# Kernel tuning notes

Measured on AMD Instinct MI355X. Metric: run time of the kernel, lower is better.

The kernel has to match this reference:

```python
import jax, jax.numpy as jnp
import numpy as np

B, S, H, I = 2, 4096, 2048, 8192
K_RATIO = 0.5
K = int(K_RATIO * I)  # 4096 kept activations per token


def setup_inputs() -> dict:
    key = jax.random.key(0)
    kx, kg, ku, kd = jax.random.split(key, 4)
    x = jax.random.normal(kx, (B, S, H), dtype=jnp.float32)
    # nn.Linear(in, out, bias=False) weight has shape [out, in]; y = x @ W.T
    Wg = jax.random.normal(kg, (I, H), dtype=jnp.float32) * (1.0 / np.sqrt(H))
    Wu = jax.random.normal(ku, (I, H), dtype=jnp.float32) * (1.0 / np.sqrt(H))
    Wd = jax.random.normal(kd, (H, I), dtype=jnp.float32) * (1.0 / np.sqrt(I))
    return {"x": x, "Wg": Wg, "Wu": Wu, "Wd": Wd}


def topk_activation(g):
    # Keep top-K entries by magnitude along the last dim, zero the rest.
    ag = jnp.abs(g)
    kth = jax.lax.top_k(ag, K)[0][..., -1:]  # [B,S,1] k-th largest |g|
    return jnp.where(ag >= kth, g, jnp.zeros_like(g))


def reference(x, Wg, Wu, Wd):
    gate = topk_activation(jnp.einsum('bsh,ih->bsi', x, Wg))  # [B,S,I] sparse
    up = jnp.einsum('bsh,ih->bsi', x, Wu)                      # [B,S,I]
    return jnp.einsum('bsi,hi->bsh', gate * up, Wd)            # [B,S,H]
```

## Files before the change

### kernel.cpp

```cpp
#include <hip/hip_runtime.h>

#define T_TOK 8192
#define HDIM  2048
#define IDIM  8192
#define KKEEP 4096
#define TCHK  4096
#define BAND  1.6e-3f
#define MAXB  192

typedef _Float16 f16x8 __attribute__((ext_vector_type(8)));
typedef float    f32x4 __attribute__((ext_vector_type(4)));
typedef ushort   u16x8 __attribute__((ext_vector_type(8)));

#define AS1 __attribute__((address_space(1)))
#define AS3 __attribute__((address_space(3)))
#define BARR asm volatile("s_barrier" ::: "memory")

__device__ __forceinline__ int swzA(int b) {
    return b ^ ((b >> 3) & 0x30) ^ ((b >> 2) & 0x40);
}

union H16 { ushort u; _Float16 h; };


__global__ void cast_f16(const float4* __restrict__ in, ushort4* __restrict__ o, long n4) {
    long stride = (long)gridDim.x * blockDim.x;
    for (long i = (long)blockIdx.x * blockDim.x + threadIdx.x; i < n4; i += stride) {
        float4 v = in[i];
        float vv[4] = {v.x, v.y, v.z, v.w};
        union { _Float16 f[4]; ushort4 u; } H;
        #pragma unroll
        for (int j = 0; j < 4; ++j) H.f[j] = (_Float16)vv[j];
        o[i] = H.u;
    }
}

#define GLOAD(src_, dst_) \
    __builtin_amdgcn_global_load_lds((const AS1 void*)(src_), (AS3 void*)(dst_), 16, 0, 0)


#define STAGE4(pA_, pB_, kt_, buf_) do { \
    char* db_ = Lc + (buf_)*32768 + wave*1024; \
    GLOAD((pA_) + aBase + (kt_) + off0, db_); \
    GLOAD((pA_) + aBase + (kt_) + off1, db_ +  8192); \
    GLOAD((pB_) + bBase + (kt_) + off2, db_ + 16384); \
    GLOAD((pB_) + bBase + (kt_) + off3, db_ + 24576); \
  } while (0)

#define RDFRAG(dstA_, dstB_, tt_) do { \
    const char* bp_ = Lc + ((tt_) & 3) * 32768; \
    _Pragma("unroll") \
    for (int m_ = 0; m_ < 8; ++m_) (dstA_)[m_] = *(const f16x8*)(bp_ + pa + m_ * 1024); \
    _Pragma("unroll") \
    for (int n_ = 0; n_ < 4; ++n_) (dstB_)[n_] = *(const f16x8*)(bp_ + pb + n_ * 1024); \
  } while (0)

#define BODY(t_, curA_, curB_, nxtA_, nxtB_) do { \
    if ((t_) + 2 < NT) asm volatile("s_waitcnt vmcnt(4)" ::: "memory"); \
    else               asm volatile("s_waitcnt vmcnt(0)" ::: "memory"); \
    BARR; \
    if ((t_) + 3 < NT) STAGE4(A0, B0, ((t_) + 3) << 5, ((t_) + 3) & 3); \
    if ((t_) + 1 < NT) RDFRAG(nxtA_, nxtB_, (t_) + 1); \
    __builtin_amdgcn_s_setprio(1); \
    _Pragma("unroll") \
    for (int m_ = 0; m_ < 8; ++m_) \
      _Pragma("unroll") \
      for (int n_ = 0; n_ < 4; ++n_) \
        acc[m_][n_] = __builtin_amdgcn_mfma_f32_16x16x32_f16((curA_)[m_], (curB_)[n_], acc[m_][n_], 0, 0, 0); \
    __builtin_amdgcn_s_setprio(0); \
  } while (0)

template <int MODE>
__global__ __launch_bounds__(512, 2) void gemm4(
    const _Float16* __restrict__ A0, const _Float16* __restrict__ B0,
    int N, int Kp, float* __restrict__ Cf, _Float16* __restrict__ Ch)
{
    __shared__ __align__(128) char Lc[131072];
    const int tid  = threadIdx.x;
    const int lane = tid & 63;
    const int wave = tid >> 6;
    const int wr = wave >> 2, wc = wave & 3;

    const int gx = gridDim.x, gy = gridDim.y;
    const int nwg = gx * gy;
    const int orig = blockIdx.y * gx + blockIdx.x;
    const int q = nwg >> 3, r = nwg & 7, xcd = orig & 7, lid = orig >> 3;
    const int wg = (xcd < r ? xcd * (q + 1) : r * (q + 1) + (xcd - r) * q) + lid;
    const int bm = wg / gy, bn = wg % gy;

    int off0, off1, off2, off3;
    {
        int o[4];
        #pragma unroll
        for (int g = 0; g < 4; ++g) {
            int p = g * 8192 + tid * 16;
            int l = swzA(p);
            int row = (l >> 6) & 255;
            int col = (l & 63) >> 1;
            o[g] = row * Kp + col;
        }
        off0 = o[0]; off1 = o[1]; off2 = o[2]; off3 = o[3];
    }
    const size_t aBase = (size_t)bm * 256 * Kp;
    const size_t bBase = (size_t)bn * 256 * Kp;

    const int l15 = lane & 15, lhi = lane >> 4;
    const int pa = swzA((wr * 128 + l15) * 64 + lhi * 16);
    const int pb = swzA(16384 + (wc * 64 + l15) * 64 + lhi * 16);

    const int NT = Kp >> 5;
    f32x4 acc[8][4] = {};
    f16x8 a0f[8], b0f[4], a1f[8], b1f[4];

    STAGE4(A0, B0, 0,  0);
    STAGE4(A0, B0, 32, 1);
    STAGE4(A0, B0, 64, 2);
    asm volatile("s_waitcnt vmcnt(8)" ::: "memory");
    BARR;
    RDFRAG(a0f, b0f, 0);

    for (int t = 0; t < NT; t += 2) {
        BODY(t,     a0f, b0f, a1f, b1f);
        BODY(t + 1, a1f, b1f, a0f, b0f);
    }

    const int r0 = bm * 256 + wr * 128 + (lane >> 4) * 4;
    const int c0 = bn * 256 + wc * 64 + (lane & 15);
    #pragma unroll
    for (int m = 0; m < 8; ++m) {
        #pragma unroll
        for (int n = 0; n < 4; ++n) {
            #pragma unroll
            for (int rr = 0; rr < 4; ++rr) {
                const size_t idx = (size_t)(r0 + m * 16 + rr) * N + (c0 + n * 16);
                if (MODE == 0) Cf[idx] = acc[m][n][rr];
                else           Ch[idx] = (_Float16)acc[m][n][rr];
            }
        }
    }
}


__global__ __launch_bounds__(256) void topk_sel(
    _Float16* __restrict__ GP, const _Float16* __restrict__ U,
    const float* __restrict__ xf, const float* __restrict__ Wgf)
{
    __shared__ ushort keys[IDIM];
    __shared__ float  xrow[HDIM];
    __shared__ unsigned char bmap[IDIM];
    __shared__ unsigned hist[256], sA_[256], sB_[256];
    __shared__ unsigned selBin, selAbove;
    __shared__ int Acnt, nbv;
    __shared__ int   bidxs[MAXB];
    __shared__ float bval[MAXB];
    __shared__ int   kflag[MAXB];

    const int tid = threadIdx.x;
    const int t = blockIdx.x;
    _Float16* grow = GP + (size_t)t * IDIM;
    const _Float16* urow = U + (size_t)t * IDIM;

    if (tid == 0) { Acnt = 0; nbv = 0; }
    for (int j8 = tid * 8; j8 < IDIM; j8 += 2048) {
        u16x8 v = *(const u16x8*)(grow + j8);
        u16x8 k;
        #pragma unroll
        for (int e = 0; e < 8; ++e) k[e] = (ushort)(v[e] & 0x7FFFu);
        *(u16x8*)(keys + j8) = k;
    }
    for (int j4 = tid; j4 < IDIM / 4; j4 += 256)
        ((unsigned*)bmap)[j4] = 0xFFFFFFFFu;
    for (int j4 = tid * 4; j4 < HDIM; j4 += 1024)
        *(float4*)(xrow + j4) = *(const float4*)(xf + (size_t)t * HDIM + j4);
    __syncthreads();

    unsigned kq = 0;
    int Krem = KKEEP;
    for (int pass = 0; pass < 2; ++pass) {
        const int shift = pass == 0 ? 7 : 0;
        const unsigned msk = pass == 0 ? 255u : 127u;
        hist[tid] = 0;
        __syncthreads();
        for (int j8 = tid * 8; j8 < IDIM; j8 += 2048) {
            u16x8 kv = *(const u16x8*)(keys + j8);
            #pragma unroll
            for (int e = 0; e < 8; ++e) {
                unsigned k = kv[e];
                bool ok = (pass == 0) || ((k >> 7) == (kq >> 7));
                if (ok) atomicAdd(&hist[(k >> shift) & msk], 1u);
            }
        }
        __syncthreads();
        sA_[tid] = hist[tid];
        __syncthreads();
        unsigned *src = sA_, *dst = sB_;
        for (int off = 1; off < 256; off <<= 1) {
            unsigned v = src[tid] + ((tid + off < 256) ? src[tid + off] : 0u);
            dst[tid] = v;
            __syncthreads();
            unsigned* tmp = src; src = dst; dst = tmp;
        }
        unsigned S  = src[tid];
        unsigned Sn = (tid < 255) ? src[tid + 1] : 0u;
        if ((int)S >= Krem && (int)Sn < Krem) { selBin = (unsigned)tid; selAbove = Sn; }
        __syncthreads();
        kq |= selBin << shift;
        Krem -= (int)selAbove;
        __syncthreads();
    }
    H16 cv; cv.u = (ushort)kq;
    const float kthf = (float)cv.h;
    const float hif = kthf + BAND;
    const float lof = kthf - BAND;

    for (int j8 = tid * 8; j8 < IDIM; j8 += 2048) {
        u16x8 kv = *(const u16x8*)(keys + j8);
        #pragma unroll
        for (int e = 0; e < 8; ++e) {
            H16 c; c.u = kv[e];
            float v = (float)c.h;
            if (v > hif) atomicAdd(&Acnt, 1);
            else if (v >= lof) {
                int s = atomicAdd(&nbv, 1);
                if (s < MAXB) { bidxs[s] = j8 + e; bmap[j8 + e] = (unsigned char)s; }
            }
        }
    }
    __syncthreads();

    const int nbc = nbv < MAXB ? nbv : MAXB;
    int R = KKEEP - Acnt;
    R = R < 0 ? 0 : (R > nbc ? nbc : R);

    const int wv = tid >> 6, ln = tid & 63;
    for (int j = wv; j < nbc; j += 4) {
        const float* wrow = Wgf + (size_t)bidxs[j] * HDIM;
        float s = 0.f;
        #pragma unroll
        for (int it = 0; it < HDIM / 256; ++it) {
            const int c = it * 256 + ln * 4;
            float4 w = *(const float4*)(wrow + c);
            float4 xv = *(const float4*)(xrow + c);
            s = fmaf(xv.x, w.x, s);
            s = fmaf(xv.y, w.y, s);
            s = fmaf(xv.z, w.z, s);
            s = fmaf(xv.w, w.w, s);
        }
        #pragma unroll
        for (int o = 32; o; o >>= 1) s += __shfl_xor(s, o);
        if (ln == 0) bval[j] = fabsf(s);
    }
    __syncthreads();

    for (int j = tid; j < nbc; j += 256) {
        int rk = 0;
        float vj = bval[j];
        for (int k = 0; k < nbc; ++k) rk += (bval[k] > vj);
        kflag[j] = (rk < R) ? 1 : 0;
    }
    __syncthreads();

    for (int j8 = tid * 8; j8 < IDIM; j8 += 2048) {
        u16x8 g8 = *(const u16x8*)(grow + j8);
        u16x8 u8 = *(const u16x8*)(urow + j8);
        u16x8 p8;
        #pragma unroll
        for (int e = 0; e < 8; ++e) {
            H16 cg; cg.u = g8[e];
            H16 cu; cu.u = u8[e];
            float g = (float)cg.h;
            float v = fabsf(g);
            bool keep;
            unsigned char s = bmap[j8 + e];
            if (s != 255)      keep = (kflag[s] != 0);
            else if (v > hif)  keep = true;
            else if (v < lof)  keep = false;
            else               keep = (v >= kthf);
            H16 cp; cp.h = keep ? (_Float16)(g * (float)cu.h) : (_Float16)0.f;
            p8[e] = cp.u;
        }
        *(u16x8*)(grow + j8) = p8;
    }
}


extern "C" void kernel_launch(void* const* d_in, const int* in_sizes, int n_in,
                              void* d_out, int out_size, void* d_ws, size_t ws_size,
                              hipStream_t stream) {
    const float* x  = (const float*)d_in[0];
    const float* Wg = (const float*)d_in[1];
    const float* Wu = (const float*)d_in[2];
    const float* Wd = (const float*)d_in[3];

    const size_t NE   = (size_t)T_TOK * HDIM;
    const size_t szH2 = NE * 2;

    char* ws = (char*)d_ws;
    _Float16* xh   = (_Float16*)ws;
    _Float16* Wgh  = (_Float16*)(ws + szH2);
    _Float16* Wu16 = (_Float16*)(ws + 2 * szH2);
    _Float16* Wd16 = (_Float16*)(ws + 3 * szH2);
    _Float16* G    = (_Float16*)(ws + 4 * szH2);
    _Float16* Uc   = (_Float16*)d_out;

    const long n4 = (long)(NE / 4);
    cast_f16<<<1024, 256, 0, stream>>>((const float4*)x,  (ushort4*)xh,   n4);
    cast_f16<<<1024, 256, 0, stream>>>((const float4*)Wg, (ushort4*)Wgh,  n4);
    cast_f16<<<1024, 256, 0, stream>>>((const float4*)Wu, (ushort4*)Wu16, n4);
    cast_f16<<<1024, 256, 0, stream>>>((const float4*)Wd, (ushort4*)Wd16, n4);

    gemm4<1><<<dim3(T_TOK / 256, IDIM / 256), 512, 0, stream>>>(
        xh, Wgh, IDIM, HDIM, nullptr, G);

    for (int c0 = 0; c0 < T_TOK; c0 += TCHK) {
        gemm4<1><<<dim3(TCHK / 256, IDIM / 256), 512, 0, stream>>>(
            xh + (size_t)c0 * HDIM, Wu16, IDIM, HDIM, nullptr, Uc);
        topk_sel<<<TCHK, 256, 0, stream>>>(
            G + (size_t)c0 * IDIM, Uc, x + (size_t)c0 * HDIM, Wg);
    }

    gemm4<0><<<dim3(T_TOK / 256, HDIM / 256), 512, 0, stream>>>(
        G, Wd16, HDIM, IDIM, (float*)d_out, nullptr);
}
```

Measured before the change: 1.243 ms.

## Shrink GEMM tile to 256x128 with four waves and double-buffered LDS

Replaces the 256x256, 8-wave GEMM with a 256x128 tile computed by 4 waves. The LDS pipeline drops from a 4-stage ring with register-level fragment double buffering to a 2-stage LDS double buffer, and each step adds an extra barrier before the refill. The point is to cut LDS use (48KB instead of 128KB) so more workgroups fit per CU and the grid gets more tiles. In exchange, global traffic per FLOP rises because the tile is smaller, and the second barrier per step may expose load latency.

```diff
diff --git a/kernel.cpp b/kernel.cpp
--- a/kernel.cpp
+++ b/kernel.cpp
@@ -39,47 +39,26 @@
     __builtin_amdgcn_global_load_lds((const AS1 void*)(src_), (AS3 void*)(dst_), 16, 0, 0)
 
 
-#define STAGE4(pA_, pB_, kt_, buf_) do { \
-    char* db_ = Lc + (buf_)*32768 + wave*1024; \
-    GLOAD((pA_) + aBase + (kt_) + off0, db_); \
-    GLOAD((pA_) + aBase + (kt_) + off1, db_ +  8192); \
-    GLOAD((pB_) + bBase + (kt_) + off2, db_ + 16384); \
-    GLOAD((pB_) + bBase + (kt_) + off3, db_ + 24576); \
+#define STAGE6(pA_, pB_, kt_, buf_) do { \
+    char* db_ = Lc + (buf_)*24576 + wave*1024; \
+    GLOAD((pA_) + aBase + (kt_) + oA0, db_); \
+    GLOAD((pA_) + aBase + (kt_) + oA1, db_ +  4096); \
+    GLOAD((pA_) + aBase + (kt_) + oA2, db_ +  8192); \
+    GLOAD((pA_) + aBase + (kt_) + oA3, db_ + 12288); \
+    GLOAD((pB_) + bBase + (kt_) + oB0, db_ + 16384); \
+    GLOAD((pB_) + bBase + (kt_) + oB1, db_ + 20480); \
   } while (0)
 
-#define RDFRAG(dstA_, dstB_, tt_) do { \
-    const char* bp_ = Lc + ((tt_) & 3) * 32768; \
-    _Pragma("unroll") \
-    for (int m_ = 0; m_ < 8; ++m_) (dstA_)[m_] = *(const f16x8*)(bp_ + pa + m_ * 1024); \
-    _Pragma("unroll") \
-    for (int n_ = 0; n_ < 4; ++n_) (dstB_)[n_] = *(const f16x8*)(bp_ + pb + n_ * 1024); \
-  } while (0)
-
-#define BODY(t_, curA_, curB_, nxtA_, nxtB_) do { \
-    if ((t_) + 2 < NT) asm volatile("s_waitcnt vmcnt(4)" ::: "memory"); \
-    else               asm volatile("s_waitcnt vmcnt(0)" ::: "memory"); \
-    BARR; \
-    if ((t_) + 3 < NT) STAGE4(A0, B0, ((t_) + 3) << 5, ((t_) + 3) & 3); \
-    if ((t_) + 1 < NT) RDFRAG(nxtA_, nxtB_, (t_) + 1); \
-    __builtin_amdgcn_s_setprio(1); \
-    _Pragma("unroll") \
-    for (int m_ = 0; m_ < 8; ++m_) \
-      _Pragma("unroll") \
-      for (int n_ = 0; n_ < 4; ++n_) \
-        acc[m_][n_] = __builtin_amdgcn_mfma_f32_16x16x32_f16((curA_)[m_], (curB_)[n_], acc[m_][n_], 0, 0, 0); \
-    __builtin_amdgcn_s_setprio(0); \
-  } while (0)
-
 template <int MODE>
-__global__ __launch_bounds__(512, 2) void gemm4(
+__global__ __launch_bounds__(256, 2) void gemm3(
     const _Float16* __restrict__ A0, const _Float16* __restrict__ B0,
     int N, int Kp, float* __restrict__ Cf, _Float16* __restrict__ Ch)
 {
-    __shared__ __align__(128) char Lc[131072];
+    __shared__ __align__(128) char Lc[49152];
     const int tid  = threadIdx.x;
     const int lane = tid & 63;
     const int wave = tid >> 6;
-    const int wr = wave >> 2, wc = wave & 3;
+    const int wr = wave >> 1, wc = wave & 1;
 
     const int gx = gridDim.x, gy = gridDim.y;
     const int nwg = gx * gy;
@@ -88,44 +67,61 @@
     const int wg = (xcd < r ? xcd * (q + 1) : r * (q + 1) + (xcd - r) * q) + lid;
     const int bm = wg / gy, bn = wg % gy;
 
-    int off0, off1, off2, off3;
+    int oA0, oA1, oA2, oA3, oB0, oB1;
     {
-        int o[4];
-        #pragma unroll
-        for (int g = 0; g < 4; ++g) {
-            int p = g * 8192 + tid * 16;
+        int o[6];
+        #pragma unroll
+        for (int g = 0; g < 6; ++g) {
+            int p = (g < 4 ? g : g - 4) * 4096 + tid * 16;
             int l = swzA(p);
-            int row = (l >> 6) & 255;
+            int row = l >> 6;
             int col = (l & 63) >> 1;
             o[g] = row * Kp + col;
         }
-        off0 = o[0]; off1 = o[1]; off2 = o[2]; off3 = o[3];
+        oA0 = o[0]; oA1 = o[1]; oA2 = o[2]; oA3 = o[3]; oB0 = o[4]; oB1 = o[5];
     }
     const size_t aBase = (size_t)bm * 256 * Kp;
-    const size_t bBase = (size_t)bn * 256 * Kp;
+    const size_t bBase = (size_t)bn * 128 * Kp;
 
     const int l15 = lane & 15, lhi = lane >> 4;
     const int pa = swzA((wr * 128 + l15) * 64 + lhi * 16);
-    const int pb = swzA(16384 + (wc * 64 + l15) * 64 + lhi * 16);
+    const int pb = 16384 + swzA((wc * 64 + l15) * 64 + lhi * 16);
 
     const int NT = Kp >> 5;
     f32x4 acc[8][4] = {};
-    f16x8 a0f[8], b0f[4], a1f[8], b1f[4];
-
-    STAGE4(A0, B0, 0,  0);
-    STAGE4(A0, B0, 32, 1);
-    STAGE4(A0, B0, 64, 2);
-    asm volatile("s_waitcnt vmcnt(8)" ::: "memory");
-    BARR;
-    RDFRAG(a0f, b0f, 0);
-
-    for (int t = 0; t < NT; t += 2) {
-        BODY(t,     a0f, b0f, a1f, b1f);
-        BODY(t + 1, a1f, b1f, a0f, b0f);
+
+    STAGE6(A0, B0, 0,  0);
+    STAGE6(A0, B0, 32, 1);
+
+    for (int t = 0; t < NT; ++t) {
+        if (t + 1 < NT) asm volatile("s_waitcnt vmcnt(6)" ::: "memory");
+        else            asm volatile("s_waitcnt vmcnt(0)" ::: "memory");
+        BARR;
+
+        const char* bp = Lc + (t & 1) * 24576;
+        f16x8 af[8], bfv[4];
+        #pragma unroll
+        for (int m = 0; m < 8; ++m) af[m]  = *(const f16x8*)(bp + pa + m * 1024);
+        #pragma unroll
+        for (int n = 0; n < 4; ++n) bfv[n] = *(const f16x8*)(bp + pb + n * 1024);
+
+        asm volatile("s_waitcnt lgkmcnt(0)" ::: "memory");
+        BARR;
+
+        if (t + 2 < NT) STAGE6(A0, B0, (t + 2) << 5, t & 1);
+
+        __builtin_amdgcn_sched_barrier(0);
+        __builtin_amdgcn_s_setprio(1);
+        #pragma unroll
+        for (int m = 0; m < 8; ++m)
+            #pragma unroll
+            for (int n = 0; n < 4; ++n)
+                acc[m][n] = __builtin_amdgcn_mfma_f32_16x16x32_f16(af[m], bfv[n], acc[m][n], 0, 0, 0);
+        __builtin_amdgcn_s_setprio(0);
     }
 
     const int r0 = bm * 256 + wr * 128 + (lane >> 4) * 4;
-    const int c0 = bn * 256 + wc * 64 + (lane & 15);
+    const int c0 = bn * 128 + wc * 64 + (lane & 15);
     #pragma unroll
     for (int m = 0; m < 8; ++m) {
         #pragma unroll
@@ -309,16 +305,16 @@
     cast_f16<<<1024, 256, 0, stream>>>((const float4*)Wu, (ushort4*)Wu16, n4);
     cast_f16<<<1024, 256, 0, stream>>>((const float4*)Wd, (ushort4*)Wd16, n4);
 
-    gemm4<1><<<dim3(T_TOK / 256, IDIM / 256), 512, 0, stream>>>(
+    gemm3<1><<<dim3(T_TOK / 256, IDIM / 128), 256, 0, stream>>>(
         xh, Wgh, IDIM, HDIM, nullptr, G);
 
     for (int c0 = 0; c0 < T_TOK; c0 += TCHK) {
-        gemm4<1><<<dim3(TCHK / 256, IDIM / 256), 512, 0, stream>>>(
+        gemm3<1><<<dim3(TCHK / 256, IDIM / 128), 256, 0, stream>>>(
             xh + (size_t)c0 * HDIM, Wu16, IDIM, HDIM, nullptr, Uc);
         topk_sel<<<TCHK, 256, 0, stream>>>(
             G + (size_t)c0 * IDIM, Uc, x + (size_t)c0 * HDIM, Wg);
     }
 
-    gemm4<0><<<dim3(T_TOK / 256, HDIM / 256), 512, 0, stream>>>(
+    gemm3<0><<<dim3(T_TOK / 256, HDIM / 128), 256, 0, stream>>>(
         G, Wd16, HDIM, IDIM, (float*)d_out, nullptr);
 }
```

Result: slower. 1.330 ms (+7.0%).
